# Optimization experiments

Hardware: AMD Instinct MI355X
Metric: run time of the kernel (lower is better)

Reference implementation:

```python
import jax, jax.numpy as jnp
import numpy as np

B, N, D, H, L = 16, 512, 256, 8, 4
DK = D // H
EPS_LN = 1e-6
EPS_ADJ = 1e-6
NEG_INF = -1e12
LAM_ATT, LAM_DIST, LAM_ADJ = 0.3, 0.3, 0.4
SLOPE = 0.1  # leaky_relu_slope


def setup_inputs() -> dict:
    key = jax.random.key(0)
    ks = jax.random.split(key, 24)
    s = 1.0 / np.sqrt(D)
    w = lambda k: jax.random.normal(k, (L, D, D), jnp.float32) * s
    b = lambda k: jax.random.normal(k, (L, D), jnp.float32) * 0.01
    return {
        "x": jax.random.normal(ks[0], (B, N, D), jnp.float32),
        "mask": jax.random.randint(ks[1], (B, N), 0, 2, jnp.int32),
        "adj_matrix": jax.random.uniform(ks[2], (B, N, N), jnp.float32),
        "distance_matrix": jax.random.uniform(ks[3], (B, N, N), jnp.float32) * 10.0,
        "edges_att": jnp.zeros((1,), jnp.float32),  # unused (use_edge_features=False)
        "Wq": w(ks[4]), "bq": b(ks[5]),
        "Wk": w(ks[6]), "bk": b(ks[7]),
        "Wv": w(ks[8]), "bv": b(ks[9]),
        "Wo": w(ks[10]), "bo": b(ks[11]),
        "Wf1": w(ks[12]), "bf1": b(ks[13]),
        "Wf2": w(ks[14]), "bf2": b(ks[15]),
        "ln1_a": jnp.ones((L, D), jnp.float32), "ln1_b": jnp.zeros((L, D), jnp.float32),
        "ln2_a": jnp.ones((L, D), jnp.float32), "ln2_b": jnp.zeros((L, D), jnp.float32),
        "lnf_a": jnp.ones((D,), jnp.float32), "lnf_b": jnp.zeros((D,), jnp.float32),
    }


def _layernorm(x, a, b):
    # torch LayerNorm here uses unbiased std and divides by (std + eps)
    m = x.mean(-1, keepdims=True)
    s = jnp.std(x, axis=-1, ddof=1, keepdims=True)
    return a * (x - m) / (s + EPS_LN) + b


def reference(x, mask, adj_matrix, distance_matrix, edges_att,
              Wq, bq, Wk, bk, Wv, bv, Wo, bo, Wf1, bf1, Wf2, bf2,
              ln1_a, ln1_b, ln2_a, ln2_b, lnf_a, lnf_b):
    maskk = (mask != 0)[:, None, :]                      # [B,1,N] key mask
    # distance kernel: softmax(-dist) with masked keys -> weight 0
    p_dist = jax.nn.softmax(jnp.where(maskk, -distance_matrix, -jnp.inf), axis=-1)  # [B,N,N]
    # row-normalized adjacency
    p_adj = adj_matrix / (adj_matrix.sum(-1, keepdims=True) + EPS_ADJ)              # [B,N,N]
    mk4 = maskk[:, :, None, :]                           # [B,1,1,N]
    inv_sqrt_dk = 1.0 / np.sqrt(DK)

    for i in range(L):
        # --- self-attention sublayer (pre-norm residual) ---
        h_in = _layernorm(x, ln1_a[i], ln1_b[i])
        q = (h_in @ Wq[i] + bq[i]).reshape(B, N, H, DK).transpose(0, 2, 1, 3)
        k = (h_in @ Wk[i] + bk[i]).reshape(B, N, H, DK).transpose(0, 2, 1, 3)
        v = (h_in @ Wv[i] + bv[i]).reshape(B, N, H, DK).transpose(0, 2, 1, 3)
        scores = jnp.einsum('bhqd,bhkd->bhqk', q, k) * inv_sqrt_dk
        p_attn = jax.nn.softmax(jnp.where(mk4, scores, NEG_INF), axis=-1)
        # three-way fused weighting over [B,H,N,N]
        p = LAM_ATT * p_attn + LAM_DIST * p_dist[:, None] + LAM_ADJ * p_adj[:, None]
        att = jnp.einsum('bhqk,bhkd->bhqd', p, v).transpose(0, 2, 1, 3).reshape(B, N, D)
        x = x + (att @ Wo[i] + bo[i])
        # --- FFN sublayer (pre-norm residual), N_dense=2 with leaky_relu ---
        h2 = _layernorm(x, ln2_a[i], ln2_b[i])
        h2 = jax.nn.leaky_relu(h2 @ Wf1[i] + bf1[i], negative_slope=SLOPE)
        h2 = jax.nn.leaky_relu(h2 @ Wf2[i] + bf2[i], negative_slope=SLOPE)
        x = x + h2

    return _layernorm(x, lnf_a, lnf_b)
```

## Files before the change

kernel.cpp:

```cpp
#include <hip/hip_runtime.h>
#include <hip/hip_bf16.h>
#include <math.h>

constexpr int kB  = 16;
constexpr int kN  = 512;
constexpr int kD  = 256;
constexpr int kH  = 8;
constexpr int kDK = 32;
constexpr int kL  = 4;

using bf16 = __hip_bfloat16;
using short8 = __attribute__((ext_vector_type(8))) short;
using floatx4 = __attribute__((ext_vector_type(4))) float;

__device__ __forceinline__ float fast_exp2(float x) {
#if __has_builtin(__builtin_amdgcn_exp2f)
    return __builtin_amdgcn_exp2f(x);
#else
    return __expf(x * 0.69314718055994531f);
#endif
}

__device__ __forceinline__ float bfs2f(short s) {
    unsigned u = ((unsigned)(unsigned short)s) << 16;
    return __uint_as_float(u);
}

__device__ __forceinline__ void gl2lds16(const bf16* g, bf16* s) {
    __builtin_amdgcn_global_load_lds(
        (const __attribute__((address_space(1))) void*)g,
        (__attribute__((address_space(3))) void*)s, 16, 0, 0);
}

__device__ __forceinline__ int swzA(int row, int inrow_byte) {
    return row * 512 + (inrow_byte ^ ((row & 7) << 4));
}

__device__ __forceinline__ float blockReduceSum(float v, float* sh) {
    #pragma unroll
    for (int o = 32; o > 0; o >>= 1) v += __shfl_down(v, o, 64);
    int lane = threadIdx.x & 63, w = threadIdx.x >> 6;
    __syncthreads();
    if (lane == 0) sh[w] = v;
    __syncthreads();
    return sh[0] + sh[1] + sh[2] + sh[3];
}

__device__ __forceinline__ float blockReduceMax(float v, float* sh) {
    #pragma unroll
    for (int o = 32; o > 0; o >>= 1) v = fmaxf(v, __shfl_down(v, o, 64));
    int lane = threadIdx.x & 63, w = threadIdx.x >> 6;
    __syncthreads();
    if (lane == 0) sh[w] = v;
    __syncthreads();
    return fmaxf(fmaxf(sh[0], sh[1]), fmaxf(sh[2], sh[3]));
}

__global__ __launch_bounds__(256) void prep_kernel(const float* __restrict__ Wq,
                                                   const float* __restrict__ Wk,
                                                   const float* __restrict__ Wv,
                                                   const float* __restrict__ Wo,
                                                   const float* __restrict__ Wf1,
                                                   const float* __restrict__ Wf2,
                                                   const float* __restrict__ bq,
                                                   const float* __restrict__ bk,
                                                   const float* __restrict__ bv,
                                                   const float* __restrict__ adj,
                                                   const float* __restrict__ dist,
                                                   const int* __restrict__ mask,
                                                   const float* __restrict__ x,
                                                   const float* __restrict__ ln1a,
                                                   const float* __restrict__ ln1b,
                                                   bf16* __restrict__ wqkv,
                                                   bf16* __restrict__ wo,
                                                   bf16* __restrict__ wf1,
                                                   bf16* __restrict__ wf2,
                                                   float* __restrict__ bcat,
                                                   bf16* __restrict__ pcb,
                                                   bf16* __restrict__ h) {
    __shared__ float tile[32][33];
    __shared__ float sh[4];
    int bid = blockIdx.x;
    int t = threadIdx.x;

    if (bid < 1536) {
        int mat = bid >> 6;
        int t6 = bid & 63;
        int tr = t6 >> 3, tc = t6 & 7;
        int layer = mat / 6, slot = mat % 6;
        const float* src =
            slot == 0 ? Wq : slot == 1 ? Wk : slot == 2 ? Wv :
            slot == 3 ? Wo : slot == 4 ? Wf1 : Wf2;
        src += (size_t)layer * kD * kD;
        bf16* dst;
        if (slot < 3) dst = wqkv + ((size_t)layer * 768 + slot * 256) * kD;
        else dst = (slot == 3 ? wo : slot == 4 ? wf1 : wf2) + (size_t)layer * kD * kD;
        int r = t >> 5, c = t & 31;
        #pragma unroll
        for (int i = 0; i < 4; i++)
            tile[r + i * 8][c] = src[(size_t)(tr * 32 + r + i * 8) * kD + tc * 32 + c];
        __syncthreads();
        #pragma unroll
        for (int i = 0; i < 4; i++)
            dst[(size_t)(tc * 32 + r + i * 8) * kD + tr * 32 + c] = bf16(tile[c][r + i * 8]);
    } else if (bid < 1548) {
        int idx = (bid - 1536) * 256 + t;
        int layer = idx / 768, j = idx % 768;
        const float* s = j < 256 ? bq : j < 512 ? bk : bv;
        bcat[idx] = s[layer * 256 + (j & 255)];
    } else if (bid < 1548 + kB * kN) {
        int row = bid - 1548;
        int b = row >> 9;
        const float* dr = dist + (size_t)row * kN;
        const float* ar = adj + (size_t)row * kN;
        const int* mr = mask + b * kN;
        float d0 = dr[t], d1 = dr[t + 256];
        float a0 = ar[t], a1 = ar[t + 256];
        int m0 = mr[t], m1 = mr[t + 256];
        const float kLog2e = 1.4426950408889634f;
        float s0 = m0 ? -d0 * kLog2e : -INFINITY;
        float s1 = m1 ? -d1 * kLog2e : -INFINITY;
        float mx = blockReduceMax(fmaxf(s0, s1), sh);
        float e0 = fast_exp2(s0 - mx);
        float e1 = fast_exp2(s1 - mx);
        float sum  = blockReduceSum(e0 + e1, sh);
        float asum = blockReduceSum(a0 + a1, sh);
        float w_d = 0.3f / sum;
        float w_a = 0.4f / (asum + 1e-6f);
        bf16* pr = pcb + (size_t)row * kN;
        pr[t]       = bf16(e0 * w_d + a0 * w_a);
        pr[t + 256] = bf16(e1 * w_d + a1 * w_a);
    } else {
        int row = bid - (1548 + kB * kN);
        float v = x[(size_t)row * kD + t];
        float m = blockReduceSum(v, sh) * (1.0f / kD);
        float dd = v - m;
        float var = blockReduceSum(dd * dd, sh) * (1.0f / (kD - 1));
        float s = sqrtf(var);
        h[(size_t)row * kD + t] = bf16(ln1a[t] * dd / (s + 1e-6f) + ln1b[t]);
    }
}

__global__ __launch_bounds__(256) void gemm_qkv(const bf16* __restrict__ A,
                                                const bf16* __restrict__ Wt,
                                                const float* __restrict__ bias,
                                                bf16* __restrict__ Cv) {
    __shared__ __align__(16) bf16 As[2][128][32];
    __shared__ __align__(16) bf16 Bs[2][64][32];
    int t = threadIdx.x;
    int m0 = blockIdx.x * 128, n0 = blockIdx.y * 64;
    int lane = t & 63, w = t >> 6, g = lane >> 4, li = lane & 15;
    int sr = lane >> 2;
    int sc = (lane & 3) * 8;

    const bf16* aSrc0 = A + (size_t)(m0 + w * 32 + sr) * kD + sc;
    const bf16* aSrc1 = aSrc0 + (size_t)16 * kD;
    const bf16* bSrc  = Wt + (size_t)(n0 + w * 16 + sr) * kD + sc;

    floatx4 zero = {0.f, 0.f, 0.f, 0.f};
    floatx4 acc[2][4];
    #pragma unroll
    for (int i = 0; i < 2; i++)
        #pragma unroll
        for (int j = 0; j < 4; j++) acc[i][j] = zero;

    auto stage = [&](int buf, int k0) {
        gl2lds16(aSrc0 + k0, &As[buf][w * 32][0]);
        gl2lds16(aSrc1 + k0, &As[buf][w * 32 + 16][0]);
        gl2lds16(bSrc  + k0, &Bs[buf][w * 16][0]);
    };

    stage(0, 0);
    __syncthreads();

    #pragma unroll
    for (int ks = 0; ks < 8; ks++) {
        const int cur = ks & 1;
        if (ks < 7) stage(cur ^ 1, (ks + 1) * 32);
        short8 af0 = *(const short8*)&As[cur][w * 32 + li][g * 8];
        short8 af1 = *(const short8*)&As[cur][w * 32 + 16 + li][g * 8];
        #pragma unroll
        for (int ct = 0; ct < 4; ct++) {
            short8 bfr = *(const short8*)&Bs[cur][ct * 16 + li][g * 8];
            acc[0][ct] = __builtin_amdgcn_mfma_f32_16x16x32_bf16(af0, bfr, acc[0][ct], 0, 0, 0);
            acc[1][ct] = __builtin_amdgcn_mfma_f32_16x16x32_bf16(af1, bfr, acc[1][ct], 0, 0, 0);
        }
        if (ks < 7) __syncthreads();
    }

    #pragma unroll
    for (int rt = 0; rt < 2; rt++) {
        #pragma unroll
        for (int ct = 0; ct < 4; ct++) {
            #pragma unroll
            for (int rr = 0; rr < 4; rr++) {
                int m = m0 + w * 32 + rt * 16 + g * 4 + rr;
                int n = n0 + ct * 16 + li;
                float v = acc[rt][ct][rr] + bias[n];
                int j = n >> 8, nn = n & 255;
                int b = m >> 9, nr = m & 511;
                int hh = nn >> 5, dk = nn & 31;
                Cv[(size_t)j * (kB * kN * kD) +
                   (((size_t)(b * kH + hh)) * kN + nr) * kDK + dk] = bf16(v);
            }
        }
    }
}

__global__ __launch_bounds__(256, 2) void attn_mfma(const bf16* __restrict__ qb,
                                                    const bf16* __restrict__ kb,
                                                    const bf16* __restrict__ vb,
                                                    const bf16* __restrict__ pcb,
                                                    const int* __restrict__ mask,
                                                    bf16* __restrict__ att) {
    __shared__ __align__(16) bf16 Vf[16 * 2 * 64 * 8];
    __shared__ __align__(16) bf16 Pbuf[4][16][136];

    int blk = blockIdx.x;
    int qt = blk & 7;
    int bh = blk >> 3;
    int b = bh >> 3;
    int h = bh & 7;
    int t = threadIdx.x;
    int lane = t & 63, w = t >> 6;
    int g = lane >> 4, li = lane & 15;

    {
        const float4* vsrc4 = (const float4*)(vb + (size_t)bh * kN * kDK);
        #pragma unroll
        for (int it = 0; it < 8; it++) {
            int idx = t + it * 256;
            float4 raw = vsrc4[idx];
            union { float4 f; bf16 hh[8]; } u; u.f = raw;
            int f0 = idx * 8;
            int n = f0 >> 5, dk0 = f0 & 31;
            int kt = n >> 5, j = n & 7, gsl = (n >> 3) & 3;
            #pragma unroll
            for (int e = 0; e < 8; e++) {
                int dk = dk0 + e;
                int dt = dk >> 4;
                int lsl = (gsl << 4) | (dk & 15);
                Vf[((((kt << 1) | dt) << 6) | lsl) * 8 + j] = u.hh[e];
            }
        }
    }
    __syncthreads();

    const bf16* qrow = qb + ((size_t)bh * kN + qt * 64 + w * 16 + li) * kDK + g * 8;
    short8 aQ = *(const short8*)qrow;
    const bf16* kbase = kb + (size_t)bh * kN * kDK;
    const int* mb = mask + b * kN;
    unsigned mbits = 0;
    #pragma unroll
    for (int tt = 0; tt < 32; tt++)
        mbits |= (unsigned)(mb[tt * 16 + li] != 0) << tt;

    floatx4 s[32];
    floatx4 zero = {0.f, 0.f, 0.f, 0.f};
    __builtin_amdgcn_s_setprio(1);
    #pragma unroll
    for (int tt = 0; tt < 32; tt++) {
        short8 bK = *(const short8*)(kbase + (size_t)(tt * 16 + li) * kDK + g * 8);
        s[tt] = __builtin_amdgcn_mfma_f32_16x16x32_bf16(aQ, bK, zero, 0, 0, 0);
    }
    __builtin_amdgcn_s_setprio(0);

    const float scale = 0.17677669529663689f * 1.4426950408889634f;
    #pragma unroll
    for (int r = 0; r < 4; r++) {
        float sum = 0.f;
        #pragma unroll
        for (int tt = 0; tt < 32; tt++) {
            bool mm = (mbits >> tt) & 1;
            float e = mm ? fast_exp2(s[tt][r] * scale) : 0.f;
            s[tt][r] = e;
            sum += e;
        }
        #pragma unroll
        for (int o = 1; o < 16; o <<= 1) sum += __shfl_xor(sum, o, 64);
        float inv = 0.3f / sum;
        #pragma unroll
        for (int tt = 0; tt < 32; tt++) s[tt][r] *= inv;
    }

    {
        const short* pcq = (const short*)(pcb + ((size_t)b * kN + qt * 64 + w * 16) * kN);
        #pragma unroll
        for (int tt = 0; tt < 32; tt++) {
            #pragma unroll
            for (int r = 0; r < 4; r++)
                s[tt][r] += bfs2f(pcq[(size_t)(g * 4 + r) * kN + tt * 16 + li]);
        }
    }

    bf16* pb = &Pbuf[w][0][0];
    floatx4 accA0 = zero, accA1 = zero;
    #pragma unroll
    for (int c = 0; c < 4; c++) {
        #pragma unroll
        for (int ttl = 0; ttl < 8; ttl++) {
            int tt = c * 8 + ttl;
            int kcol = ttl * 16 + li;
            #pragma unroll
            for (int r = 0; r < 4; r++)
                pb[(g * 4 + r) * 136 + kcol] = bf16(s[tt][r]);
        }
        __builtin_amdgcn_s_setprio(1);
        #pragma unroll
        for (int k2 = 0; k2 < 4; k2++) {
            int ktile = c * 4 + k2;
            short8 aP  = *(const short8*)(pb + li * 136 + k2 * 32 + g * 8);
            short8 bV0 = *(const short8*)(&Vf[((ktile * 2 + 0) * 64 + lane) * 8]);
            short8 bV1 = *(const short8*)(&Vf[((ktile * 2 + 1) * 64 + lane) * 8]);
            accA0 = __builtin_amdgcn_mfma_f32_16x16x32_bf16(aP, bV0, accA0, 0, 0, 0);
            accA1 = __builtin_amdgcn_mfma_f32_16x16x32_bf16(aP, bV1, accA1, 0, 0, 0);
        }
        __builtin_amdgcn_s_setprio(0);
    }

    #pragma unroll
    for (int r = 0; r < 4; r++) {
        size_t row = (size_t)b * kN + qt * 64 + w * 16 + g * 4 + r;
        bf16* arow = att + row * kD + h * kDK;
        arow[li]      = bf16(accA0[r]);
        arow[16 + li] = bf16(accA1[r]);
    }
}

__device__ __forceinline__ void gemm_phase16(const char* asb, const bf16* __restrict__ Wt,
                                             bf16 (*Bs)[256][32],
                                             int w, int lane, int g, int li,
                                             floatx4 acc[4]) {
    auto stageB = [&](int buf, int k0) {
        #pragma unroll
        for (int c = 0; c < 4; c++) {
            int row = w * 64 + c * 16;
            gl2lds16(Wt + (size_t)(row + (lane >> 2)) * kD + k0 + (lane & 3) * 8,
                     &Bs[buf][row][0]);
        }
    };
    stageB(0, 0);
    #pragma unroll
    for (int ks = 0; ks < 8; ks++) {
        const int cur = ks & 1;
        __builtin_amdgcn_sched_barrier(0);
        if (ks < 7) {
            stageB(cur ^ 1, (ks + 1) * 32);
            asm volatile("s_waitcnt vmcnt(4)" ::: "memory");
        } else {
            asm volatile("s_waitcnt vmcnt(0)" ::: "memory");
        }
        __builtin_amdgcn_sched_barrier(0);
        short8 af0 = *(const short8*)(asb + swzA(li, (ks * 4 + g) << 4));
        __builtin_amdgcn_s_setprio(1);
        #pragma unroll
        for (int ct = 0; ct < 4; ct++) {
            short8 bfr = *(const short8*)&Bs[cur][w * 64 + ct * 16 + li][g * 8];
            acc[ct] = __builtin_amdgcn_mfma_f32_16x16x32_bf16(af0, bfr, acc[ct], 0, 0, 0);
        }
        __builtin_amdgcn_s_setprio(0);
    }
}

__device__ __forceinline__ void row_ln_stats16(floatx4 xv[4],
                                               float (*psumS)[16], float (*psqS)[16],
                                               int w, int g, int li,
                                               float outMean[4], float outInv[4]) {
    #pragma unroll
    for (int rr = 0; rr < 4; rr++) {
        float s4 = 0.f, q4 = 0.f;
        #pragma unroll
        for (int ct = 0; ct < 4; ct++) {
            float v = xv[ct][rr];
            s4 += v;
            q4 += v * v;
        }
        #pragma unroll
        for (int o = 1; o < 16; o <<= 1) {
            s4 += __shfl_xor(s4, o, 64);
            q4 += __shfl_xor(q4, o, 64);
        }
        int row = g * 4 + rr;
        if (li == 0) { psumS[w][row] = s4; psqS[w][row] = q4; }
    }
    __syncthreads();
    #pragma unroll
    for (int rr = 0; rr < 4; rr++) {
        int row = g * 4 + rr;
        float s  = psumS[0][row] + psumS[1][row] + psumS[2][row] + psumS[3][row];
        float ss = psqS[0][row]  + psqS[1][row]  + psqS[2][row]  + psqS[3][row];
        float mean = s * (1.0f / kD);
        float var = (ss - (float)kD * mean * mean) * (1.0f / (kD - 1));
        outMean[rr] = mean;
        outInv[rr] = 1.0f / (sqrtf(var) + 1e-6f);
    }
}

template <bool LAST>
__global__ __launch_bounds__(256) void block_tail(const bf16* __restrict__ A,
                                                  const bf16* __restrict__ Wot,
                                                  const float* __restrict__ bo,
                                                  const float* __restrict__ resid,
                                                  const bf16* __restrict__ W1t,
                                                  const float* __restrict__ b1,
                                                  const bf16* __restrict__ W2t,
                                                  const float* __restrict__ b2,
                                                  const float* __restrict__ ln2a,
                                                  const float* __restrict__ ln2b,
                                                  const float* __restrict__ lnna,
                                                  const float* __restrict__ lnnb,
                                                  float* __restrict__ xcOut,
                                                  bf16* __restrict__ hOut,
                                                  float* __restrict__ fOut) {
    __shared__ __align__(16) bf16 As[16][256];
    __shared__ __align__(16) bf16 Bs[2][256][32];
    __shared__ float psumS[4][16], psqS[4][16];

    int t = threadIdx.x;
    int m0 = blockIdx.x * 16;
    int lane = t & 63, w = t >> 6, g = lane >> 4, li = lane & 15;

    {
        int r = t >> 4;
        int cbase = (t & 15) * 2;
        const bf16* src = A + (size_t)(m0 + r) * kD;
        char* asb = (char*)&As[0][0];
        #pragma unroll
        for (int c = 0; c < 2; c++) {
            int chunk = cbase + c;
            short8 v = *(const short8*)(src + chunk * 8);
            *(short8*)(asb + swzA(r, chunk << 4)) = v;
        }
    }
    __syncthreads();

    floatx4 zero = {0.f, 0.f, 0.f, 0.f};
    floatx4 acc[4];
    #pragma unroll
    for (int j = 0; j < 4; j++) acc[j] = zero;

    gemm_phase16((const char*)&As[0][0], Wot, Bs, w, lane, g, li, acc);

    floatx4 xs[4];
    #pragma unroll
    for (int ct = 0; ct < 4; ct++) {
        #pragma unroll
        for (int rr = 0; rr < 4; rr++) {
            int m = m0 + g * 4 + rr;
            int n = w * 64 + ct * 16 + li;
            float xv = resid[(size_t)m * kD + n] + acc[ct][rr] + bo[n];
            xs[ct][rr] = xv;
            acc[ct][rr] = xv;
        }
    }

    float mean[4], inv[4];
    row_ln_stats16(acc, psumS, psqS, w, g, li, mean, inv);
    {
        char* asb = (char*)&As[0][0];
        #pragma unroll
        for (int ct = 0; ct < 4; ct++) {
            #pragma unroll
            for (int rr = 0; rr < 4; rr++) {
                int row = g * 4 + rr;
                int col = w * 64 + ct * 16 + li;
                float y = ln2a[col] * (xs[ct][rr] - mean[rr]) * inv[rr] + ln2b[col];
                *(bf16*)(asb + swzA(row, col * 2)) = bf16(y);
            }
        }
    }
    __syncthreads();

    #pragma unroll
    for (int j = 0; j < 4; j++) acc[j] = zero;

    gemm_phase16((const char*)&As[0][0], W1t, Bs, w, lane, g, li, acc);

    __syncthreads();

    {
        char* asb = (char*)&As[0][0];
        #pragma unroll
        for (int ct = 0; ct < 4; ct++) {
            #pragma unroll
            for (int rr = 0; rr < 4; rr++) {
                int row = g * 4 + rr;
                int col = w * 64 + ct * 16 + li;
                float v = acc[ct][rr] + b1[col];
                v = v > 0.f ? v : 0.1f * v;
                *(bf16*)(asb + swzA(row, col * 2)) = bf16(v);
            }
        }
    }
    __syncthreads();

    #pragma unroll
    for (int j = 0; j < 4; j++) acc[j] = zero;

    gemm_phase16((const char*)&As[0][0], W2t, Bs, w, lane, g, li, acc);

    #pragma unroll
    for (int ct = 0; ct < 4; ct++) {
        #pragma unroll
        for (int rr = 0; rr < 4; rr++) {
            int m = m0 + g * 4 + rr;
            int n = w * 64 + ct * 16 + li;
            float v = acc[ct][rr] + b2[n];
            v = v > 0.f ? v : 0.1f * v;
            float xv = xs[ct][rr] + v;
            if (!LAST) xcOut[(size_t)m * kD + n] = xv;
            acc[ct][rr] = xv;
        }
    }

    row_ln_stats16(acc, psumS, psqS, w, g, li, mean, inv);

    #pragma unroll
    for (int ct = 0; ct < 4; ct++) {
        #pragma unroll
        for (int rr = 0; rr < 4; rr++) {
            int m = m0 + g * 4 + rr;
            int n = w * 64 + ct * 16 + li;
            float y = lnna[n] * (acc[ct][rr] - mean[rr]) * inv[rr] + lnnb[n];
            if (LAST) fOut[(size_t)m * kD + n] = y;
            else      hOut[(size_t)m * kD + n] = bf16(y);
        }
    }
}

extern "C" void kernel_launch(void* const* d_in, const int* in_sizes, int n_in,
                              void* d_out, int out_size, void* d_ws, size_t ws_size,
                              hipStream_t stream) {
    const float* x    = (const float*)d_in[0];
    const int*   mask = (const int*)d_in[1];
    const float* adj  = (const float*)d_in[2];
    const float* dist = (const float*)d_in[3];
    const float* Wq = (const float*)d_in[5];  const float* bq = (const float*)d_in[6];
    const float* Wk = (const float*)d_in[7];  const float* bk = (const float*)d_in[8];
    const float* Wv = (const float*)d_in[9];  const float* bv = (const float*)d_in[10];
    const float* Wo = (const float*)d_in[11]; const float* bo = (const float*)d_in[12];
    const float* Wf1 = (const float*)d_in[13]; const float* bf1 = (const float*)d_in[14];
    const float* Wf2 = (const float*)d_in[15]; const float* bf2 = (const float*)d_in[16];
    const float* ln1a = (const float*)d_in[17]; const float* ln1b = (const float*)d_in[18];
    const float* ln2a = (const float*)d_in[19]; const float* ln2b = (const float*)d_in[20];
    const float* lnfa = (const float*)d_in[21]; const float* lnfb = (const float*)d_in[22];

    const size_t rows = (size_t)kB * kN;
    const size_t actN = rows * kD;

    char* wsb = (char*)d_ws;
    bf16*  pcb   = (bf16*)wsb;  wsb += (size_t)kB * kN * kN * sizeof(bf16);
    float* xc    = (float*)wsb; wsb += actN * sizeof(float);
    bf16*  h     = (bf16*)wsb;  wsb += actN * sizeof(bf16);
    bf16*  attb  = (bf16*)wsb;  wsb += actN * sizeof(bf16);
    bf16*  qkvb  = (bf16*)wsb;  wsb += 3 * actN * sizeof(bf16);
    bf16*  wqkv  = (bf16*)wsb;  wsb += (size_t)kL * 768 * kD * sizeof(bf16);
    bf16*  wo_t  = (bf16*)wsb;  wsb += (size_t)kL * kD * kD * sizeof(bf16);
    bf16*  wf1_t = (bf16*)wsb;  wsb += (size_t)kL * kD * kD * sizeof(bf16);
    bf16*  wf2_t = (bf16*)wsb;  wsb += (size_t)kL * kD * kD * sizeof(bf16);
    float* bcat  = (float*)wsb; wsb += (size_t)kL * 768 * sizeof(float);

    prep_kernel<<<1548 + 2 * kB * kN, 256, 0, stream>>>(
        Wq, Wk, Wv, Wo, Wf1, Wf2, bq, bk, bv, adj, dist, mask, x, ln1a, ln1b,
        wqkv, wo_t, wf1_t, wf2_t, bcat, pcb, h);

    dim3 gQKV(64, 12);
    const int g16 = rows / 16;
    for (int i = 0; i < kL; i++) {
        const size_t bOff = (size_t)i * kD;
        const size_t wOff = (size_t)i * kD * kD;
        const float* xin = (i == 0) ? x : xc;
        gemm_qkv<<<gQKV, 256, 0, stream>>>(h, wqkv + (size_t)i * 768 * kD,
                                           bcat + (size_t)i * 768, qkvb);
        attn_mfma<<<kB * kH * (kN / 64), 256, 0, stream>>>(qkvb, qkvb + actN,
                                                           qkvb + 2 * actN,
                                                           pcb, mask, attb);
        if (i < kL - 1) {
            block_tail<false><<<g16, 256, 0, stream>>>(
                attb, wo_t + wOff, bo + bOff, xin,
                wf1_t + wOff, bf1 + bOff, wf2_t + wOff, bf2 + bOff,
                ln2a + bOff, ln2b + bOff,
                ln1a + (size_t)(i + 1) * kD, ln1b + (size_t)(i + 1) * kD,
                xc, h, nullptr);
        } else {
            block_tail<true><<<g16, 256, 0, stream>>>(
                attb, wo_t + wOff, bo + bOff, xin,
                wf1_t + wOff, bf1 + bOff, wf2_t + wOff, bf2 + bOff,
                ln2a + bOff, ln2b + bOff, lnfa, lnfb,
                nullptr, nullptr, (float*)d_out);
        }
    }
}
```

Before: 347.2 us.

## Write V in attention-ready fragment layout from the QKV GEMM epilogue

The QKV GEMM blocks that produce V now transpose their tile through shared memory (a union reusing the staging buffers) and write V directly in the MFMA fragment-permuted layout the attention kernel expects. The attention kernel then loads V with direct global-to-LDS 16-byte copies instead of per-element scattered LDS stores. This removes an expensive scatter/shuffle in each attention block, in exchange for extra LDS traffic and syncs in the V-producing GEMM blocks.

```diff
diff --git a/kernel.cpp b/kernel.cpp
--- a/kernel.cpp
+++ b/kernel.cpp
@@ -145,8 +145,10 @@
                                                 const bf16* __restrict__ Wt,
                                                 const float* __restrict__ bias,
                                                 bf16* __restrict__ Cv) {
-    __shared__ __align__(16) bf16 As[2][128][32];
-    __shared__ __align__(16) bf16 Bs[2][64][32];
+    __shared__ __align__(16) union {
+        struct { bf16 As[2][128][32]; bf16 Bs[2][64][32]; } g;
+        bf16 tr[64][136];
+    } sm;
     int t = threadIdx.x;
     int m0 = blockIdx.x * 128, n0 = blockIdx.y * 64;
     int lane = t & 63, w = t >> 6, g = lane >> 4, li = lane & 15;
@@ -165,9 +167,9 @@
         for (int j = 0; j < 4; j++) acc[i][j] = zero;
 
     auto stage = [&](int buf, int k0) {
-        gl2lds16(aSrc0 + k0, &As[buf][w * 32][0]);
-        gl2lds16(aSrc1 + k0, &As[buf][w * 32 + 16][0]);
-        gl2lds16(bSrc  + k0, &Bs[buf][w * 16][0]);
+        gl2lds16(aSrc0 + k0, &sm.g.As[buf][w * 32][0]);
+        gl2lds16(aSrc1 + k0, &sm.g.As[buf][w * 32 + 16][0]);
+        gl2lds16(bSrc  + k0, &sm.g.Bs[buf][w * 16][0]);
     };
 
     stage(0, 0);
@@ -177,32 +179,64 @@
     for (int ks = 0; ks < 8; ks++) {
         const int cur = ks & 1;
         if (ks < 7) stage(cur ^ 1, (ks + 1) * 32);
-        short8 af0 = *(const short8*)&As[cur][w * 32 + li][g * 8];
-        short8 af1 = *(const short8*)&As[cur][w * 32 + 16 + li][g * 8];
+        short8 af0 = *(const short8*)&sm.g.As[cur][w * 32 + li][g * 8];
+        short8 af1 = *(const short8*)&sm.g.As[cur][w * 32 + 16 + li][g * 8];
         #pragma unroll
         for (int ct = 0; ct < 4; ct++) {
-            short8 bfr = *(const short8*)&Bs[cur][ct * 16 + li][g * 8];
+            short8 bfr = *(const short8*)&sm.g.Bs[cur][ct * 16 + li][g * 8];
             acc[0][ct] = __builtin_amdgcn_mfma_f32_16x16x32_bf16(af0, bfr, acc[0][ct], 0, 0, 0);
             acc[1][ct] = __builtin_amdgcn_mfma_f32_16x16x32_bf16(af1, bfr, acc[1][ct], 0, 0, 0);
         }
         if (ks < 7) __syncthreads();
     }
 
-    #pragma unroll
-    for (int rt = 0; rt < 2; rt++) {
-        #pragma unroll
-        for (int ct = 0; ct < 4; ct++) {
+    if (blockIdx.y < 8) {
+        #pragma unroll
+        for (int rt = 0; rt < 2; rt++) {
             #pragma unroll
-            for (int rr = 0; rr < 4; rr++) {
-                int m = m0 + w * 32 + rt * 16 + g * 4 + rr;
-                int n = n0 + ct * 16 + li;
-                float v = acc[rt][ct][rr] + bias[n];
-                int j = n >> 8, nn = n & 255;
-                int b = m >> 9, nr = m & 511;
-                int hh = nn >> 5, dk = nn & 31;
-                Cv[(size_t)j * (kB * kN * kD) +
-                   (((size_t)(b * kH + hh)) * kN + nr) * kDK + dk] = bf16(v);
+            for (int ct = 0; ct < 4; ct++) {
+                #pragma unroll
+                for (int rr = 0; rr < 4; rr++) {
+                    int m = m0 + w * 32 + rt * 16 + g * 4 + rr;
+                    int n = n0 + ct * 16 + li;
+                    float v = acc[rt][ct][rr] + bias[n];
+                    int j = n >> 8, nn = n & 255;
+                    int b = m >> 9, nr = m & 511;
+                    int hh = nn >> 5, dk = nn & 31;
+                    Cv[(size_t)j * (kB * kN * kD) +
+                       (((size_t)(b * kH + hh)) * kN + nr) * kDK + dk] = bf16(v);
+                }
             }
+        }
+    } else {
+        __syncthreads();
+        #pragma unroll
+        for (int rt = 0; rt < 2; rt++) {
+            #pragma unroll
+            for (int ct = 0; ct < 4; ct++) {
+                #pragma unroll
+                for (int rr = 0; rr < 4; rr++) {
+                    int mloc = w * 32 + rt * 16 + g * 4 + rr;
+                    int ncol = ct * 16 + li;
+                    sm.tr[ncol][mloc] = bf16(acc[rt][ct][rr] + bias[n0 + ncol]);
+                }
+            }
+        }
+        __syncthreads();
+        int b = m0 >> 9;
+        int nrbase = m0 & 511;
+        bf16* vtb2 = Cv + 2 * (size_t)(kB * kN * kD);
+        #pragma unroll
+        for (int it = 0; it < 4; it++) {
+            int idx = t + it * 256;
+            int rid = idx >> 4;
+            int cid = (idx & 15) * 8;
+            int nn = (n0 + rid) & 255;
+            int hh = nn >> 5, dk = nn & 31;
+            int nr = nrbase + cid;
+            int chunk = (nr >> 5) * 128 + (dk >> 4) * 64 + ((nr >> 3) & 3) * 16 + (dk & 15);
+            bf16* dst = vtb2 + ((size_t)(b * kH + hh) * 2048 + chunk) * 8;
+            *(short8*)dst = *(const short8*)&sm.tr[rid][cid];
         }
     }
 }
@@ -226,22 +260,11 @@
     int g = lane >> 4, li = lane & 15;
 
     {
-        const float4* vsrc4 = (const float4*)(vb + (size_t)bh * kN * kDK);
+        const bf16* vsrc = vb + (size_t)bh * (2048 * 8);
         #pragma unroll
         for (int it = 0; it < 8; it++) {
-            int idx = t + it * 256;
-            float4 raw = vsrc4[idx];
-            union { float4 f; bf16 hh[8]; } u; u.f = raw;
-            int f0 = idx * 8;
-            int n = f0 >> 5, dk0 = f0 & 31;
-            int kt = n >> 5, j = n & 7, gsl = (n >> 3) & 3;
-            #pragma unroll
-            for (int e = 0; e < 8; e++) {
-                int dk = dk0 + e;
-                int dt = dk >> 4;
-                int lsl = (gsl << 4) | (dk & 15);
-                Vf[((((kt << 1) | dt) << 6) | lsl) * 8 + j] = u.hh[e];
-            }
+            int cb = it * 256 + w * 64;
+            gl2lds16(vsrc + (size_t)(cb + lane) * 8, &Vf[cb * 8]);
         }
     }
     __syncthreads();
```

Measured after the change: 346.5 us. Within noise of the previous version (-0.2%).
